# Kernel tuning notes

Measured on AMD Instinct MI355X. Metric: run time of the kernel, lower is better.

## Reference

```python
import jax, jax.numpy as jnp
import numpy as np

D_MODEL = 1024
N_HEADS = 16
HEAD_DIM = D_MODEL // N_HEADS  # 64
BATCH, SEQ = 2, 2048
MASK_FILL = -1000000000.0


def setup_inputs() -> dict:
    key = jax.random.key(0)
    ks = jax.random.split(key, 13)
    s = 1.0 / np.sqrt(D_MODEL)
    inp = {
        "q": jax.random.normal(ks[0], (BATCH, SEQ, D_MODEL), jnp.float32),
        "k": jax.random.normal(ks[1], (BATCH, SEQ, D_MODEL), jnp.float32),
        "v": jax.random.normal(ks[2], (BATCH, SEQ, D_MODEL), jnp.float32),
        "mask": jax.random.randint(ks[3], (BATCH, 1, SEQ, SEQ), 0, 2, jnp.int32),
        "Wq": jax.random.normal(ks[4], (D_MODEL, D_MODEL), jnp.float32) * s,
        "bq": jax.random.normal(ks[5], (D_MODEL,), jnp.float32) * s,
        "Wk": jax.random.normal(ks[6], (D_MODEL, D_MODEL), jnp.float32) * s,
        "bk": jax.random.normal(ks[7], (D_MODEL,), jnp.float32) * s,
        "Wv": jax.random.normal(ks[8], (D_MODEL, D_MODEL), jnp.float32) * s,
        "bv": jax.random.normal(ks[9], (D_MODEL,), jnp.float32) * s,
        "Wo": jax.random.normal(ks[10], (D_MODEL, D_MODEL), jnp.float32) * s,
        "bo": jax.random.normal(ks[11], (D_MODEL,), jnp.float32) * s,
    }
    return inp


def reference(q, k, v, mask, Wq, bq, Wk, bk, Wv, bv, Wo, bo):
    batch, seq, feat = q.shape
    # Linear projections (torch Linear: x @ W.T + b)
    qp = q @ Wq.T + bq
    kp = k @ Wk.T + bk
    vp = v @ Wv.T + bv

    def split(x):
        # (B, S, D) -> (B, H, S, Dh)
        return x.reshape(batch, seq, N_HEADS, HEAD_DIM).swapaxes(1, 2)

    qh, kh, vh = split(qp), split(kp), split(vp)

    # (B, H, S, S) score matrix, scaled
    score = jnp.einsum("bhqd,bhkd->bhqk", qh, kh) / jnp.sqrt(
        jnp.asarray(HEAD_DIM, qh.dtype))
    score = jnp.where(mask == 0, jnp.asarray(MASK_FILL, score.dtype), score)
    attn = jax.nn.softmax(score, axis=-1)
    out = jnp.einsum("bhqk,bhkd->bhqd", attn, vh)  # (B, H, S, Dh)
    joint = out.swapaxes(1, 2).reshape(batch, seq, feat)
    return joint @ Wo.T + bo
```

## Files before the change

### kernel.cpp

```cpp
#include <hip/hip_runtime.h>

typedef unsigned short u16;
typedef unsigned long long u64;
typedef float f32x4 __attribute__((ext_vector_type(4)));
typedef __bf16 bf16x4 __attribute__((ext_vector_type(4)));
typedef __bf16 bf16x8 __attribute__((ext_vector_type(8)));
typedef u16 u16x8 __attribute__((ext_vector_type(8)));

#define QSCALE 0.18033688011112042f

__device__ __forceinline__ u16 f2bf(float f) {
  unsigned int u = __float_as_uint(f);
  u += 0x7fffu + ((u >> 16) & 1u);
  return (u16)(u >> 16);
}

__device__ __forceinline__ void async16(const void* g, void* l) {
  __builtin_amdgcn_global_load_lds(
      (__attribute__((address_space(1))) void*)g,
      (__attribute__((address_space(3))) void*)l,
      16, 0, 0);
}

__device__ __forceinline__ f32x4 mfma16(bf16x8 a, bf16x8 b, f32x4 c) {
  return __builtin_amdgcn_mfma_f32_16x16x32_bf16(a, b, c, 0, 0, 0);
}

struct CvtArgs {
  const float* src[7];
  u16* dst[7];
};

__global__ __launch_bounds__(256) void cvt_kernel(CvtArgs a) {
  int z = blockIdx.z;
  int n = (z < 3) ? 4194304 : 1048576;
  int base = (blockIdx.x * 256 + threadIdx.x) * 8;
  if (base >= n) return;
  const float* s = a.src[z] + base;
  f32x4 x0 = *(const f32x4*)s;
  f32x4 x1 = *(const f32x4*)(s + 4);
  u16x8 pk;
  pk[0]=f2bf(x0[0]); pk[1]=f2bf(x0[1]); pk[2]=f2bf(x0[2]); pk[3]=f2bf(x0[3]);
  pk[4]=f2bf(x1[0]); pk[5]=f2bf(x1[1]); pk[6]=f2bf(x1[2]); pk[7]=f2bf(x1[3]);
  *(u16x8*)(a.dst[z] + base) = pk;
}

__global__ __launch_bounds__(256) void pack_mask_kernel(
    const int* __restrict__ mask, u64* __restrict__ pm) {
  int idx = blockIdx.x * 256 + threadIdx.x;
  const int4* src = (const int4*)(mask + (size_t)idx * 64);
  u64 bits = 0ull;
#pragma unroll
  for (int j = 0; j < 16; ++j) {
    int4 v = src[j];
    if (v.x) bits |= 1ull << (4 * j + 0);
    if (v.y) bits |= 1ull << (4 * j + 1);
    if (v.z) bits |= 1ull << (4 * j + 2);
    if (v.w) bits |= 1ull << (4 * j + 3);
  }
  pm[idx] = bits;
}

__device__ __forceinline__ void gemm_body(const u16* __restrict__ A,
                                          const u16* __restrict__ W,
                                          const float* __restrict__ bias,
                                          void* __restrict__ outraw, int mode,
                                          float oscale) {
  alignas(16) __shared__ u16 lA[128 * 32];
  alignas(16) __shared__ u16 lB[128 * 32];
  const int tid = threadIdx.x;
  const int lane = tid & 63, wv = tid >> 6;
  const int wm = wv >> 1, wn = wv & 1;
  const int m0 = blockIdx.y * 128, n0 = blockIdx.x * 128;
  const int l15 = lane & 15, quad = lane >> 4;
  const int srow = lane >> 2;
  const int scol = (lane & 3) * 8;

  f32x4 acc[4][4] = {};

  for (int k0 = 0; k0 < 1024; k0 += 32) {
#pragma unroll
    for (int t = 0; t < 2; ++t) {
      int rb = (wv * 2 + t) * 16;
      async16(A + (size_t)(m0 + rb + srow) * 1024 + k0 + scol, (char*)lA + rb * 64);
      async16(W + (size_t)(n0 + rb + srow) * 1024 + k0 + scol, (char*)lB + rb * 64);
    }
    __syncthreads();
    bf16x8 af[4], bfr[4];
#pragma unroll
    for (int i = 0; i < 4; ++i) {
      af[i]  = *(const bf16x8*)(lA + (wm * 64 + i * 16 + l15) * 32 + quad * 8);
      bfr[i] = *(const bf16x8*)(lB + (wn * 64 + i * 16 + l15) * 32 + quad * 8);
    }
#pragma unroll
    for (int i = 0; i < 4; ++i)
#pragma unroll
      for (int j = 0; j < 4; ++j)
        acc[i][j] = mfma16(af[i], bfr[j], acc[i][j]);
    __syncthreads();
  }

#pragma unroll
  for (int i = 0; i < 4; ++i) {
    int mbase = m0 + wm * 64 + i * 16 + quad * 4;
#pragma unroll
    for (int j = 0; j < 4; ++j) {
      int n = n0 + wn * 64 + j * 16 + l15;
      float bv = bias[n];
#pragma unroll
      for (int r = 0; r < 4; ++r) {
        int m = mbase + r;
        float val = (acc[i][j][r] + bv) * oscale;
        if (mode == 0) {
          int b = m >> 11, s = m & 2047, h = n >> 6, dh = n & 63;
          ((u16*)outraw)[((((size_t)b * 16 + h) * 2048 + s) << 6) + dh] = f2bf(val);
        } else if (mode == 1) {
          int b = m >> 11, s = m & 2047, h = n >> 6, dh = n & 63;
          ((u16*)outraw)[((((size_t)b * 16 + h) * 64 + dh) << 11) + s] = f2bf(val);
        } else {
          ((float*)outraw)[(size_t)m * 1024 + n] = val;
        }
      }
    }
  }
}

__global__ __launch_bounds__(256) void gemm_qkv_kernel(
    const u16* __restrict__ qb, const u16* __restrict__ kb, const u16* __restrict__ vb,
    const u16* __restrict__ Wqb, const float* __restrict__ bq,
    const u16* __restrict__ Wkb, const float* __restrict__ bk,
    const u16* __restrict__ Wvb, const float* __restrict__ bv,
    u16* __restrict__ qp, u16* __restrict__ kp, u16* __restrict__ vt) {
  if (blockIdx.z == 0)      gemm_body(qb, Wqb, bq, qp, 0, QSCALE);
  else if (blockIdx.z == 1) gemm_body(kb, Wkb, bk, kp, 0, 1.0f);
  else                      gemm_body(vb, Wvb, bv, vt, 1, 1.0f);
}

__global__ __launch_bounds__(256) void gemm_o_kernel(
    const u16* __restrict__ joint, const u16* __restrict__ Wob,
    const float* __restrict__ bo, float* __restrict__ out) {
  gemm_body(joint, Wob, bo, out, 2, 1.0f);
}

__global__ __launch_bounds__(256, 2) void attn_kernel(
    const u16* __restrict__ qp, const u16* __restrict__ kp,
    const u16* __restrict__ vt, const u64* __restrict__ pm,
    u16* __restrict__ joint) {
  alignas(16) __shared__ u16 kbuf[2][4096];
  alignas(16) __shared__ u16 vbuf[2][4096];
  alignas(16) __shared__ u16 pbuf[4][2][1024];

  const int tid = threadIdx.x, lane = tid & 63, wv = tid >> 6;
  const int quad = lane >> 4, l15 = lane & 15;
  const int q0 = blockIdx.x * 128;
  const int h = blockIdx.y, b = blockIdx.z;
  const size_t head_off = ((size_t)b * 16 + h) * 2048 * 64;
  const u16* Qh = qp + head_off;
  const u16* Kh = kp + head_off;
  const u16* Vh = vt + head_off;
  const int qr0 = q0 + wv * 32 + l15;
  const u64* pmq = pm + ((size_t)b * 2048 + qr0) * 32;

  bf16x8 qf[2][2];
#pragma unroll
  for (int g = 0; g < 2; ++g) {
    const u16* qrow = Qh + (size_t)(qr0 + g * 16) * 64 + quad * 8;
    qf[g][0] = *(const bf16x8*)(qrow);
    qf[g][1] = *(const bf16x8*)(qrow + 32);
  }

  const int sd0 = tid, sd1 = 256 + tid;
  const int snt0 = sd0 >> 7, shalf0 = (sd0 >> 6) & 1, sl60 = sd0 & 63;
  const int snt1 = sd1 >> 7, shalf1 = (sd1 >> 6) & 1, sl61 = sd1 & 63;
  const u16* kg0 = Kh + (size_t)(snt0 * 16 + (sl60 & 15)) * 64 + shalf0 * 32 + (sl60 >> 4) * 8;
  const u16* kg1 = Kh + (size_t)(snt1 * 16 + (sl61 & 15)) * 64 + shalf1 * 32 + (sl61 >> 4) * 8;
  const int vb0 = sd0 >> 6, vb1 = sd1 >> 6;
  const u16* vg0 = Vh + (size_t)((vb0 >> 1) * 16 + (sl60 & 15)) * 2048 + (vb0 & 1) * 32 + (sl60 >> 4) * 8;
  const u16* vg1 = Vh + (size_t)((vb1 >> 1) * 16 + (sl61 & 15)) * 2048 + (vb1 & 1) * 32 + (sl61 >> 4) * 8;

  f32x4 O[2][4] = {};
  f32x4 lacc[2] = {};

  async16(kg0, (char*)kbuf[0] + sd0 * 16);
  async16(kg1, (char*)kbuf[0] + sd1 * 16);
  async16(vg0, (char*)vbuf[0] + sd0 * 16);
  async16(vg1, (char*)vbuf[0] + sd1 * 16);

  for (int kt = 0; kt < 32; ++kt) {
    __syncthreads();

    if (kt != 31) {
      const size_t kadv = (size_t)(kt + 1) * 4096;
      const int vadv = (kt + 1) * 64;
      char* kd = (char*)kbuf[(kt + 1) & 1];
      char* vd = (char*)vbuf[(kt + 1) & 1];
      async16(kg0 + kadv, kd + sd0 * 16);
      async16(kg1 + kadv, kd + sd1 * 16);
      async16(vg0 + vadv, vd + sd0 * 16);
      async16(vg1 + vadv, vd + sd1 * 16);
    }

    u64 w0 = pmq[kt], w1 = pmq[kt + 512];
    const u16* kc = kbuf[kt & 1];
    const u16* vc = vbuf[kt & 1];

    bf16x8 kf[8];
#pragma unroll
    for (int nt = 0; nt < 4; ++nt) {
      kf[2 * nt]     = *(const bf16x8*)(kc + nt * 1024 + lane * 8);
      kf[2 * nt + 1] = *(const bf16x8*)(kc + nt * 1024 + 512 + lane * 8);
    }

    f32x4 S[2][4];
#pragma unroll
    for (int g = 0; g < 2; ++g)
#pragma unroll
      for (int nt = 0; nt < 4; ++nt) {
        f32x4 z = {};
        z = mfma16(kf[2 * nt], qf[g][0], z);
        S[g][nt] = mfma16(kf[2 * nt + 1], qf[g][1], z);
      }

#pragma unroll
    for (int g = 0; g < 2; ++g) {
      u64 word = g ? w1 : w0;
      unsigned int wlo = (unsigned int)word, whi = (unsigned int)(word >> 32);
#pragma unroll
      for (int nt = 0; nt < 4; ++nt) {
        unsigned int hw = (nt < 2) ? wlo : whi;
        unsigned int nib = hw >> ((nt & 1) * 16 + quad * 4);
#pragma unroll
        for (int r = 0; r < 4; ++r) {
          float pe = __builtin_amdgcn_exp2f(S[g][nt][r]);
          S[g][nt][r] = ((nib >> r) & 1u) ? pe : 0.f;
        }
        lacc[g] += S[g][nt];
        bf16x4 pv = __builtin_convertvector(S[g][nt], bf16x4);
        int t4 = 4 * nt + quad;
        int ks = t4 >> 3, qd = (t4 & 7) >> 1;
        u16* pw = pbuf[wv][g] + ks * 512 + qd * 128 + l15 * 8 + (t4 & 1) * 4;
        *(u64*)pw = *(const u64*)&pv;
      }
    }

    bf16x8 vf[8];
#pragma unroll
    for (int nt = 0; nt < 4; ++nt) {
      vf[2 * nt]     = *(const bf16x8*)(vc + (nt * 2) * 512 + lane * 8);
      vf[2 * nt + 1] = *(const bf16x8*)(vc + (nt * 2 + 1) * 512 + lane * 8);
    }
    asm volatile("s_waitcnt lgkmcnt(0)" ::: "memory");

#pragma unroll
    for (int ks = 0; ks < 2; ++ks) {
      bf16x8 pf0 = *(const bf16x8*)(pbuf[wv][0] + ks * 512 + lane * 8);
      bf16x8 pf1 = *(const bf16x8*)(pbuf[wv][1] + ks * 512 + lane * 8);
#pragma unroll
      for (int nt = 0; nt < 4; ++nt) {
        O[0][nt] = mfma16(vf[2 * nt + ks], pf0, O[0][nt]);
        O[1][nt] = mfma16(vf[2 * nt + ks], pf1, O[1][nt]);
      }
    }
  }

#pragma unroll
  for (int g = 0; g < 2; ++g) {
    float l = (lacc[g][0] + lacc[g][1]) + (lacc[g][2] + lacc[g][3]);
    l += __shfl_xor(l, 16, 64);
    l += __shfl_xor(l, 32, 64);
    float inv = 1.0f / l;
    size_t row_off = ((size_t)b * 2048 + qr0 + g * 16) * 1024 + h * 64;
#pragma unroll
    for (int nt = 0; nt < 4; ++nt) {
      f32x4 ov = O[g][nt] * inv;
      bf16x4 obv = __builtin_convertvector(ov, bf16x4);
      *(u64*)(joint + row_off + nt * 16 + quad * 4) = *(const u64*)&obv;
    }
  }
}

extern "C" void kernel_launch(void* const* d_in, const int* in_sizes, int n_in,
                              void* d_out, int out_size, void* d_ws, size_t ws_size,
                              hipStream_t stream) {
  const float* q  = (const float*)d_in[0];
  const float* k  = (const float*)d_in[1];
  const float* v  = (const float*)d_in[2];
  const int* mask = (const int*)d_in[3];
  const float* Wq = (const float*)d_in[4];
  const float* bq = (const float*)d_in[5];
  const float* Wk = (const float*)d_in[6];
  const float* bk = (const float*)d_in[7];
  const float* Wv = (const float*)d_in[8];
  const float* bv = (const float*)d_in[9];
  const float* Wo = (const float*)d_in[10];
  const float* bo = (const float*)d_in[11];
  float* out = (float*)d_out;

  u16* w = (u16*)d_ws;
  u16* qp    = w;
  u16* kp    = w + 4194304;
  u16* vt    = w + 8388608;
  u16* qb    = w + 12582912;
  u16* kb    = w + 16777216;
  u16* vb    = w + 20971520;
  u16* Wqb   = w + 25165824;
  u16* Wkb   = w + 26214400;
  u16* Wvb   = w + 27262976;
  u16* Wob   = w + 28311552;
  u64* pm    = (u64*)(w + 29360128);
  u16* joint = qb;

  CvtArgs ca;
  ca.src[0] = q;  ca.dst[0] = qb;
  ca.src[1] = k;  ca.dst[1] = kb;
  ca.src[2] = v;  ca.dst[2] = vb;
  ca.src[3] = Wq; ca.dst[3] = Wqb;
  ca.src[4] = Wk; ca.dst[4] = Wkb;
  ca.src[5] = Wv; ca.dst[5] = Wvb;
  ca.src[6] = Wo; ca.dst[6] = Wob;

  pack_mask_kernel<<<dim3(512), dim3(256), 0, stream>>>(mask, pm);
  cvt_kernel<<<dim3(2048, 1, 7), dim3(256), 0, stream>>>(ca);
  gemm_qkv_kernel<<<dim3(8, 32, 3), dim3(256), 0, stream>>>(
      qb, kb, vb, Wqb, bq, Wkb, bk, Wvb, bv, qp, kp, vt);
  attn_kernel<<<dim3(16, 16, 2), dim3(256), 0, stream>>>(qp, kp, vt, pm, joint);
  gemm_o_kernel<<<dim3(8, 32, 1), dim3(256), 0, stream>>>(joint, Wob, bo, out);
}
```

Before: 287.3 us.

## Software-pipeline PV MFMAs one tile behind QK and raise wave priority

Restructures the attention inner loop so the P·V matrix multiplies for tile kt-1 are issued together with the Q·K multiplies for tile kt. V and P fragments are carried in registers across iterations, and a tail step finishes the last tile. The barrier moves to the end of each iteration, and s_setprio wraps the MFMA block so that block gets higher wave priority. The aim is to overlap the exp/mask/LDS-store phase with matrix-core work, at the cost of more live registers and possible occupancy loss.

```diff
diff --git a/kernel.cpp b/kernel.cpp
--- a/kernel.cpp
+++ b/kernel.cpp
@@ -181,14 +181,16 @@
   f32x4 O[2][4] = {};
   f32x4 lacc[2] = {};
 
+  bf16x8 vfp[8];
+  bf16x8 pfp[2][2];
+
   async16(kg0, (char*)kbuf[0] + sd0 * 16);
   async16(kg1, (char*)kbuf[0] + sd1 * 16);
   async16(vg0, (char*)vbuf[0] + sd0 * 16);
   async16(vg1, (char*)vbuf[0] + sd1 * 16);
+  __syncthreads();
 
   for (int kt = 0; kt < 32; ++kt) {
-    __syncthreads();
-
     if (kt != 31) {
       const size_t kadv = (size_t)(kt + 1) * 4096;
       const int vadv = (kt + 1) * 64;
@@ -211,15 +213,33 @@
       kf[2 * nt + 1] = *(const bf16x8*)(kc + nt * 1024 + 512 + lane * 8);
     }
 
+    __builtin_amdgcn_s_setprio(1);
+    if (kt != 0) {
+#pragma unroll
+      for (int ks = 0; ks < 2; ++ks)
+#pragma unroll
+        for (int nt = 0; nt < 4; ++nt) {
+          O[0][nt] = mfma16(vfp[2 * nt + ks], pfp[ks][0], O[0][nt]);
+          O[1][nt] = mfma16(vfp[2 * nt + ks], pfp[ks][1], O[1][nt]);
+        }
+    }
+
+    const f32x4 fz = {};
     f32x4 S[2][4];
 #pragma unroll
     for (int g = 0; g < 2; ++g)
 #pragma unroll
       for (int nt = 0; nt < 4; ++nt) {
-        f32x4 z = {};
-        z = mfma16(kf[2 * nt], qf[g][0], z);
+        f32x4 z = mfma16(kf[2 * nt], qf[g][0], fz);
         S[g][nt] = mfma16(kf[2 * nt + 1], qf[g][1], z);
       }
+    __builtin_amdgcn_s_setprio(0);
+
+#pragma unroll
+    for (int nt = 0; nt < 4; ++nt) {
+      vfp[2 * nt]     = *(const bf16x8*)(vc + (nt * 2) * 512 + lane * 8);
+      vfp[2 * nt + 1] = *(const bf16x8*)(vc + (nt * 2 + 1) * 512 + lane * 8);
+    }
 
 #pragma unroll
     for (int g = 0; g < 2; ++g) {
@@ -243,25 +263,24 @@
       }
     }
 
-    bf16x8 vf[8];
+    asm volatile("s_waitcnt lgkmcnt(0)" ::: "memory");
+
+#pragma unroll
+    for (int ks = 0; ks < 2; ++ks) {
+      pfp[ks][0] = *(const bf16x8*)(pbuf[wv][0] + ks * 512 + lane * 8);
+      pfp[ks][1] = *(const bf16x8*)(pbuf[wv][1] + ks * 512 + lane * 8);
+    }
+
+    __syncthreads();
+  }
+
+#pragma unroll
+  for (int ks = 0; ks < 2; ++ks)
 #pragma unroll
     for (int nt = 0; nt < 4; ++nt) {
-      vf[2 * nt]     = *(const bf16x8*)(vc + (nt * 2) * 512 + lane * 8);
-      vf[2 * nt + 1] = *(const bf16x8*)(vc + (nt * 2 + 1) * 512 + lane * 8);
-    }
-    asm volatile("s_waitcnt lgkmcnt(0)" ::: "memory");
-
-#pragma unroll
-    for (int ks = 0; ks < 2; ++ks) {
-      bf16x8 pf0 = *(const bf16x8*)(pbuf[wv][0] + ks * 512 + lane * 8);
-      bf16x8 pf1 = *(const bf16x8*)(pbuf[wv][1] + ks * 512 + lane * 8);
-#pragma unroll
-      for (int nt = 0; nt < 4; ++nt) {
-        O[0][nt] = mfma16(vf[2 * nt + ks], pf0, O[0][nt]);
-        O[1][nt] = mfma16(vf[2 * nt + ks], pf1, O[1][nt]);
-      }
-    }
-  }
+      O[0][nt] = mfma16(vfp[2 * nt + ks], pfp[ks][0], O[0][nt]);
+      O[1][nt] = mfma16(vfp[2 * nt + ks], pfp[ks][1], O[1][nt]);
+    }
 
 #pragma unroll
   for (int g = 0; g < 2; ++g) {
```

Result: no change. 288.3 us (+0.3%).

## Software-pipeline attention loop so QK^T of next tile overlaps softmax and PV

Applied to the files above, without the earlier changes.

Restructures the attention inner loop into a two-stage software pipeline. The QK^T MFMAs for tile kt are interleaved with the exp/mask softmax of tile kt-1, and PV for the previous tile runs while the V fragments for the current tile are loaded. The point is to overlap matrix-core work with the VALU exp work and LDS traffic that were serialized before. The cost is doubled S and V register buffers, which raises VGPR pressure and may reduce occupancy, plus explicit prologue and epilogue code.

```diff
diff --git a/kernel.cpp b/kernel.cpp
--- a/kernel.cpp
+++ b/kernel.cpp
@@ -180,88 +180,129 @@
 
   f32x4 O[2][4] = {};
   f32x4 lacc[2] = {};
+  const f32x4 fz = {};
+
+  f32x4 SA[2][4], SB[2][4];
+  bf16x8 vfA[8], vfB[8];
+  u64 wA0, wA1, wB0, wB1;
+
+#define SM_CHUNK(SP, WLO, WHI, g, nt)                                          \
+  do {                                                                         \
+    unsigned int hw_ = ((nt) < 2) ? (WLO) : (WHI);                             \
+    unsigned int nib_ = hw_ >> (((nt) & 1) * 16 + quad * 4);                   \
+    _Pragma("unroll") for (int r_ = 0; r_ < 4; ++r_) {                         \
+      float pe_ = __builtin_amdgcn_exp2f(SP[g][nt][r_]);                       \
+      SP[g][nt][r_] = ((nib_ >> r_) & 1u) ? pe_ : 0.f;                         \
+    }                                                                          \
+    lacc[g] += SP[g][nt];                                                      \
+    bf16x4 pv_ = __builtin_convertvector(SP[g][nt], bf16x4);                   \
+    int t4_ = 4 * (nt) + quad;                                                 \
+    int ks_ = t4_ >> 3, qd_ = (t4_ & 7) >> 1;                                  \
+    u16* pw_ = pbuf[wv][g] + ks_ * 512 + qd_ * 128 + l15 * 8 + (t4_ & 1) * 4;  \
+    *(u64*)pw_ = *(const u64*)&pv_;                                            \
+  } while (0)
+
+#define ATTN_STEP(SC, SP, VC, VP, WC0, WC1, WP0, WP1, KT)                      \
+  do {                                                                         \
+    const int kt_ = (KT);                                                      \
+    if (kt_ != 31) {                                                           \
+      const size_t kadv_ = (size_t)(kt_ + 1) * 4096;                           \
+      const int vadv_ = (kt_ + 1) * 64;                                        \
+      char* kd_ = (char*)kbuf[(kt_ + 1) & 1];                                  \
+      char* vd_ = (char*)vbuf[(kt_ + 1) & 1];                                  \
+      async16(kg0 + kadv_, kd_ + sd0 * 16);                                    \
+      async16(kg1 + kadv_, kd_ + sd1 * 16);                                    \
+      async16(vg0 + vadv_, vd_ + sd0 * 16);                                    \
+      async16(vg1 + vadv_, vd_ + sd1 * 16);                                    \
+    }                                                                          \
+    WC0 = pmq[kt_]; WC1 = pmq[kt_ + 512];                                      \
+    const u16* kc_ = kbuf[kt_ & 1];                                            \
+    const u16* vc_ = vbuf[kt_ & 1];                                            \
+    unsigned int plo0_ = (unsigned int)(WP0), phi0_ = (unsigned int)((WP0) >> 32); \
+    unsigned int plo1_ = (unsigned int)(WP1), phi1_ = (unsigned int)((WP1) >> 32); \
+    _Pragma("unroll") for (int nt = 0; nt < 4; ++nt) {                         \
+      bf16x8 k0_ = *(const bf16x8*)(kc_ + nt * 1024 + lane * 8);               \
+      bf16x8 k1_ = *(const bf16x8*)(kc_ + nt * 1024 + 512 + lane * 8);         \
+      f32x4 z0_ = mfma16(k0_, qf[0][0], fz);                                   \
+      SC[0][nt] = mfma16(k1_, qf[0][1], z0_);                                  \
+      f32x4 z1_ = mfma16(k0_, qf[1][0], fz);                                   \
+      SC[1][nt] = mfma16(k1_, qf[1][1], z1_);                                  \
+      SM_CHUNK(SP, plo0_, phi0_, 0, nt);                                       \
+      SM_CHUNK(SP, plo1_, phi1_, 1, nt);                                       \
+    }                                                                          \
+    asm volatile("s_waitcnt lgkmcnt(0)" ::: "memory");                         \
+    _Pragma("unroll") for (int ks = 0; ks < 2; ++ks) {                         \
+      bf16x8 pf0_ = *(const bf16x8*)(pbuf[wv][0] + ks * 512 + lane * 8);       \
+      bf16x8 pf1_ = *(const bf16x8*)(pbuf[wv][1] + ks * 512 + lane * 8);       \
+      _Pragma("unroll") for (int nt = 0; nt < 4; ++nt) {                       \
+        O[0][nt] = mfma16(VP[2 * nt + ks], pf0_, O[0][nt]);                    \
+        O[1][nt] = mfma16(VP[2 * nt + ks], pf1_, O[1][nt]);                    \
+      }                                                                        \
+    }                                                                          \
+    _Pragma("unroll") for (int nt = 0; nt < 4; ++nt) {                         \
+      VC[2 * nt]     = *(const bf16x8*)(vc_ + (nt * 2) * 512 + lane * 8);      \
+      VC[2 * nt + 1] = *(const bf16x8*)(vc_ + (nt * 2 + 1) * 512 + lane * 8);  \
+    }                                                                          \
+    __syncthreads();                                                           \
+  } while (0)
 
   async16(kg0, (char*)kbuf[0] + sd0 * 16);
   async16(kg1, (char*)kbuf[0] + sd1 * 16);
   async16(vg0, (char*)vbuf[0] + sd0 * 16);
   async16(vg1, (char*)vbuf[0] + sd1 * 16);
-
-  for (int kt = 0; kt < 32; ++kt) {
-    __syncthreads();
-
-    if (kt != 31) {
-      const size_t kadv = (size_t)(kt + 1) * 4096;
-      const int vadv = (kt + 1) * 64;
-      char* kd = (char*)kbuf[(kt + 1) & 1];
-      char* vd = (char*)vbuf[(kt + 1) & 1];
-      async16(kg0 + kadv, kd + sd0 * 16);
-      async16(kg1 + kadv, kd + sd1 * 16);
-      async16(vg0 + vadv, vd + sd0 * 16);
-      async16(vg1 + vadv, vd + sd1 * 16);
-    }
-
-    u64 w0 = pmq[kt], w1 = pmq[kt + 512];
-    const u16* kc = kbuf[kt & 1];
-    const u16* vc = vbuf[kt & 1];
-
-    bf16x8 kf[8];
+  __syncthreads();
+
+  async16(kg0 + 4096, (char*)kbuf[1] + sd0 * 16);
+  async16(kg1 + 4096, (char*)kbuf[1] + sd1 * 16);
+  async16(vg0 + 64,   (char*)vbuf[1] + sd0 * 16);
+  async16(vg1 + 64,   (char*)vbuf[1] + sd1 * 16);
+
+  wA0 = pmq[0]; wA1 = pmq[512];
+#pragma unroll
+  for (int nt = 0; nt < 4; ++nt) {
+    bf16x8 k0_ = *(const bf16x8*)(kbuf[0] + nt * 1024 + lane * 8);
+    bf16x8 k1_ = *(const bf16x8*)(kbuf[0] + nt * 1024 + 512 + lane * 8);
+    f32x4 z0_ = mfma16(k0_, qf[0][0], fz);
+    SA[0][nt] = mfma16(k1_, qf[0][1], z0_);
+    f32x4 z1_ = mfma16(k0_, qf[1][0], fz);
+    SA[1][nt] = mfma16(k1_, qf[1][1], z1_);
+  }
+#pragma unroll
+  for (int nt = 0; nt < 4; ++nt) {
+    vfA[2 * nt]     = *(const bf16x8*)(vbuf[0] + (nt * 2) * 512 + lane * 8);
+    vfA[2 * nt + 1] = *(const bf16x8*)(vbuf[0] + (nt * 2 + 1) * 512 + lane * 8);
+  }
+  __syncthreads();
+
+  for (int it = 0; it < 15; ++it) {
+    ATTN_STEP(SB, SA, vfB, vfA, wB0, wB1, wA0, wA1, 2 * it + 1);
+    ATTN_STEP(SA, SB, vfA, vfB, wA0, wA1, wB0, wB1, 2 * it + 2);
+  }
+  ATTN_STEP(SB, SA, vfB, vfA, wB0, wB1, wA0, wA1, 31);
+
+  {
+    unsigned int plo0_ = (unsigned int)wB0, phi0_ = (unsigned int)(wB0 >> 32);
+    unsigned int plo1_ = (unsigned int)wB1, phi1_ = (unsigned int)(wB1 >> 32);
 #pragma unroll
     for (int nt = 0; nt < 4; ++nt) {
-      kf[2 * nt]     = *(const bf16x8*)(kc + nt * 1024 + lane * 8);
-      kf[2 * nt + 1] = *(const bf16x8*)(kc + nt * 1024 + 512 + lane * 8);
-    }
-
-    f32x4 S[2][4];
-#pragma unroll
-    for (int g = 0; g < 2; ++g)
+      SM_CHUNK(SB, plo0_, phi0_, 0, nt);
+      SM_CHUNK(SB, plo1_, phi1_, 1, nt);
+    }
+    asm volatile("s_waitcnt lgkmcnt(0)" ::: "memory");
+#pragma unroll
+    for (int ks = 0; ks < 2; ++ks) {
+      bf16x8 pf0_ = *(const bf16x8*)(pbuf[wv][0] + ks * 512 + lane * 8);
+      bf16x8 pf1_ = *(const bf16x8*)(pbuf[wv][1] + ks * 512 + lane * 8);
 #pragma unroll
       for (int nt = 0; nt < 4; ++nt) {
-        f32x4 z = {};
-        z = mfma16(kf[2 * nt], qf[g][0], z);
-        S[g][nt] = mfma16(kf[2 * nt + 1], qf[g][1], z);
+        O[0][nt] = mfma16(vfB[2 * nt + ks], pf0_, O[0][nt]);
+        O[1][nt] = mfma16(vfB[2 * nt + ks], pf1_, O[1][nt]);
       }
-
-#pragma unroll
-    for (int g = 0; g < 2; ++g) {
-      u64 word = g ? w1 : w0;
-      unsigned int wlo = (unsigned int)word, whi = (unsigned int)(word >> 32);
-#pragma unroll
-      for (int nt = 0; nt < 4; ++nt) {
-        unsigned int hw = (nt < 2) ? wlo : whi;
-        unsigned int nib = hw >> ((nt & 1) * 16 + quad * 4);
-#pragma unroll
-        for (int r = 0; r < 4; ++r) {
-          float pe = __builtin_amdgcn_exp2f(S[g][nt][r]);
-          S[g][nt][r] = ((nib >> r) & 1u) ? pe : 0.f;
-        }
-        lacc[g] += S[g][nt];
-        bf16x4 pv = __builtin_convertvector(S[g][nt], bf16x4);
-        int t4 = 4 * nt + quad;
-        int ks = t4 >> 3, qd = (t4 & 7) >> 1;
-        u16* pw = pbuf[wv][g] + ks * 512 + qd * 128 + l15 * 8 + (t4 & 1) * 4;
-        *(u64*)pw = *(const u64*)&pv;
-      }
-    }
-
-    bf16x8 vf[8];
-#pragma unroll
-    for (int nt = 0; nt < 4; ++nt) {
-      vf[2 * nt]     = *(const bf16x8*)(vc + (nt * 2) * 512 + lane * 8);
-      vf[2 * nt + 1] = *(const bf16x8*)(vc + (nt * 2 + 1) * 512 + lane * 8);
-    }
-    asm volatile("s_waitcnt lgkmcnt(0)" ::: "memory");
-
-#pragma unroll
-    for (int ks = 0; ks < 2; ++ks) {
-      bf16x8 pf0 = *(const bf16x8*)(pbuf[wv][0] + ks * 512 + lane * 8);
-      bf16x8 pf1 = *(const bf16x8*)(pbuf[wv][1] + ks * 512 + lane * 8);
-#pragma unroll
-      for (int nt = 0; nt < 4; ++nt) {
-        O[0][nt] = mfma16(vf[2 * nt + ks], pf0, O[0][nt]);
-        O[1][nt] = mfma16(vf[2 * nt + ks], pf1, O[1][nt]);
-      }
-    }
-  }
+    }
+  }
+
+#undef ATTN_STEP
+#undef SM_CHUNK
 
 #pragma unroll
   for (int g = 0; g < 2; ++g) {
```

Result: no change. 285.6 us (-0.6%).

## Halve attention query tile per block to raise occupancy and block count

Applied to the files above, without the earlier changes.

Each wave now handles 16 query rows instead of 32, so each block covers 64 queries, and the grid doubles to 1024 blocks. The launch bound is raised to 4 blocks per CU and register/LDS use drops, aiming for more waves in flight and better CU coverage. In exchange, each K/V tile loaded into shared memory is reused by half as many queries, doubling K/V global traffic and the async-load overhead per unit of work. Softmax still skips max subtraction, relying on the prescaled scores staying in range.

```diff
diff --git a/kernel.cpp b/kernel.cpp
--- a/kernel.cpp
+++ b/kernel.cpp
@@ -142,31 +142,30 @@
   gemm_body(joint, Wob, bo, out, 2, 1.0f);
 }
 
-__global__ __launch_bounds__(256, 2) void attn_kernel(
+__global__ __launch_bounds__(256, 4) void attn_kernel(
     const u16* __restrict__ qp, const u16* __restrict__ kp,
     const u16* __restrict__ vt, const u64* __restrict__ pm,
     u16* __restrict__ joint) {
   alignas(16) __shared__ u16 kbuf[2][4096];
   alignas(16) __shared__ u16 vbuf[2][4096];
-  alignas(16) __shared__ u16 pbuf[4][2][1024];
+  alignas(16) __shared__ u16 pbuf[4][1024];
 
   const int tid = threadIdx.x, lane = tid & 63, wv = tid >> 6;
   const int quad = lane >> 4, l15 = lane & 15;
-  const int q0 = blockIdx.x * 128;
+  const int q0 = blockIdx.x * 64;
   const int h = blockIdx.y, b = blockIdx.z;
   const size_t head_off = ((size_t)b * 16 + h) * 2048 * 64;
   const u16* Qh = qp + head_off;
   const u16* Kh = kp + head_off;
   const u16* Vh = vt + head_off;
-  const int qr0 = q0 + wv * 32 + l15;
-  const u64* pmq = pm + ((size_t)b * 2048 + qr0) * 32;
-
-  bf16x8 qf[2][2];
-#pragma unroll
-  for (int g = 0; g < 2; ++g) {
-    const u16* qrow = Qh + (size_t)(qr0 + g * 16) * 64 + quad * 8;
-    qf[g][0] = *(const bf16x8*)(qrow);
-    qf[g][1] = *(const bf16x8*)(qrow + 32);
+  const int qr = q0 + wv * 16 + l15;
+  const u64* pmq = pm + ((size_t)b * 2048 + qr) * 32;
+
+  bf16x8 qf[2];
+  {
+    const u16* qrow = Qh + (size_t)qr * 64 + quad * 8;
+    qf[0] = *(const bf16x8*)(qrow);
+    qf[1] = *(const bf16x8*)(qrow + 32);
   }
 
   const int sd0 = tid, sd1 = 256 + tid;
@@ -178,8 +177,9 @@
   const u16* vg0 = Vh + (size_t)((vb0 >> 1) * 16 + (sl60 & 15)) * 2048 + (vb0 & 1) * 32 + (sl60 >> 4) * 8;
   const u16* vg1 = Vh + (size_t)((vb1 >> 1) * 16 + (sl61 & 15)) * 2048 + (vb1 & 1) * 32 + (sl61 >> 4) * 8;
 
-  f32x4 O[2][4] = {};
-  f32x4 lacc[2] = {};
+  f32x4 O[4] = {};
+  f32x4 lacc = {};
+  const f32x4 fz = {};
 
   async16(kg0, (char*)kbuf[0] + sd0 * 16);
   async16(kg1, (char*)kbuf[0] + sd1 * 16);
@@ -200,7 +200,7 @@
       async16(vg1 + vadv, vd + sd1 * 16);
     }
 
-    u64 w0 = pmq[kt], w1 = pmq[kt + 512];
+    u64 word = pmq[kt];
     const u16* kc = kbuf[kt & 1];
     const u16* vc = vbuf[kt & 1];
 
@@ -211,19 +211,14 @@
       kf[2 * nt + 1] = *(const bf16x8*)(kc + nt * 1024 + 512 + lane * 8);
     }
 
-    f32x4 S[2][4];
-#pragma unroll
-    for (int g = 0; g < 2; ++g)
-#pragma unroll
-      for (int nt = 0; nt < 4; ++nt) {
-        f32x4 z = {};
-        z = mfma16(kf[2 * nt], qf[g][0], z);
-        S[g][nt] = mfma16(kf[2 * nt + 1], qf[g][1], z);
-      }
-
-#pragma unroll
-    for (int g = 0; g < 2; ++g) {
-      u64 word = g ? w1 : w0;
+    f32x4 S[4];
+#pragma unroll
+    for (int nt = 0; nt < 4; ++nt) {
+      f32x4 z = mfma16(kf[2 * nt], qf[0], fz);
+      S[nt] = mfma16(kf[2 * nt + 1], qf[1], z);
+    }
+
+    {
       unsigned int wlo = (unsigned int)word, whi = (unsigned int)(word >> 32);
 #pragma unroll
       for (int nt = 0; nt < 4; ++nt) {
@@ -231,14 +226,14 @@
         unsigned int nib = hw >> ((nt & 1) * 16 + quad * 4);
 #pragma unroll
         for (int r = 0; r < 4; ++r) {
-          float pe = __builtin_amdgcn_exp2f(S[g][nt][r]);
-          S[g][nt][r] = ((nib >> r) & 1u) ? pe : 0.f;
+          float pe = __builtin_amdgcn_exp2f(S[nt][r]);
+          S[nt][r] = ((nib >> r) & 1u) ? pe : 0.f;
         }
-        lacc[g] += S[g][nt];
-        bf16x4 pv = __builtin_convertvector(S[g][nt], bf16x4);
+        lacc += S[nt];
+        bf16x4 pv = __builtin_convertvector(S[nt], bf16x4);
         int t4 = 4 * nt + quad;
         int ks = t4 >> 3, qd = (t4 & 7) >> 1;
-        u16* pw = pbuf[wv][g] + ks * 512 + qd * 128 + l15 * 8 + (t4 & 1) * 4;
+        u16* pw = pbuf[wv] + ks * 512 + qd * 128 + l15 * 8 + (t4 & 1) * 4;
         *(u64*)pw = *(const u64*)&pv;
       }
     }
@@ -253,26 +248,22 @@
 
 #pragma unroll
     for (int ks = 0; ks < 2; ++ks) {
-      bf16x8 pf0 = *(const bf16x8*)(pbuf[wv][0] + ks * 512 + lane * 8);
-      bf16x8 pf1 = *(const bf16x8*)(pbuf[wv][1] + ks * 512 + lane * 8);
-#pragma unroll
-      for (int nt = 0; nt < 4; ++nt) {
-        O[0][nt] = mfma16(vf[2 * nt + ks], pf0, O[0][nt]);
-        O[1][nt] = mfma16(vf[2 * nt + ks], pf1, O[1][nt]);
-      }
-    }
-  }
-
-#pragma unroll
-  for (int g = 0; g < 2; ++g) {
-    float l = (lacc[g][0] + lacc[g][1]) + (lacc[g][2] + lacc[g][3]);
+      bf16x8 pf = *(const bf16x8*)(pbuf[wv] + ks * 512 + lane * 8);
+#pragma unroll
+      for (int nt = 0; nt < 4; ++nt)
+        O[nt] = mfma16(vf[2 * nt + ks], pf, O[nt]);
+    }
+  }
+
+  {
+    float l = (lacc[0] + lacc[1]) + (lacc[2] + lacc[3]);
     l += __shfl_xor(l, 16, 64);
     l += __shfl_xor(l, 32, 64);
     float inv = 1.0f / l;
-    size_t row_off = ((size_t)b * 2048 + qr0 + g * 16) * 1024 + h * 64;
+    size_t row_off = ((size_t)b * 2048 + qr) * 1024 + h * 64;
 #pragma unroll
     for (int nt = 0; nt < 4; ++nt) {
-      f32x4 ov = O[g][nt] * inv;
+      f32x4 ov = O[nt] * inv;
       bf16x4 obv = __builtin_convertvector(ov, bf16x4);
       *(u64*)(joint + row_off + nt * 16 + quad * 4) = *(const u64*)&obv;
     }
@@ -323,6 +314,6 @@
   cvt_kernel<<<dim3(2048, 1, 7), dim3(256), 0, stream>>>(ca);
   gemm_qkv_kernel<<<dim3(8, 32, 3), dim3(256), 0, stream>>>(
       qb, kb, vb, Wqb, bq, Wkb, bk, Wvb, bv, qp, kp, vt);
-  attn_kernel<<<dim3(16, 16, 2), dim3(256), 0, stream>>>(qp, kp, vt, pm, joint);
+  attn_kernel<<<dim3(32, 16, 2), dim3(256), 0, stream>>>(qp, kp, vt, pm, joint);
   gemm_o_kernel<<<dim3(8, 32, 1), dim3(256), 0, stream>>>(joint, Wob, bo, out);
 }
```

New measurement: 300.4 us. 4.6% more time.
